# Performance work log

Measured on AMD Instinct MI355X. Metric: run time of the kernel, lower is better.

The kernel has to match this reference:

```python
import jax, jax.numpy as jnp
import numpy as np

L = 768          # temporal feature length
C_IN = 2048      # feature channels
NA = 10          # anchor scales per position
NC = 21          # num classes (20 + bg)
PRE_NMS = 1024   # pre-NMS top-k
POST_NMS = 128   # fixed proposal count after NMS
NMS_THR = 0.7
SCALE = 1.0      # cfg.Process.new_dilation*new_cluster/Frame
ANCHOR_SIZES = np.array([2., 4., 5., 6., 8., 9., 10., 12., 14., 16.], np.float32)


def _conv(x, w, b, pad=0):
    # x: [N,C,T], w: [O,I,K]
    y = jax.lax.conv_general_dilated(x, w, (1,), [(pad, pad)],
                                     dimension_numbers=('NCH', 'OIH', 'NCH'))
    return y + b[None, :, None]


def _lin(x, w, b):
    return x @ w.T + b


def _forward(feature, p):
    f = _conv(feature, p['w1f'], p['b1f'], 1)
    f = _conv(f, p['w2f'], p['b2f'], 1)
    x = _conv(f, p['wc1'], p['bc1'], 0)                      # [1,512,L]
    # SegmentProposal tower (relu only after conv4, as in source)
    h = _conv(x, p['sp1w'], p['sp1b'], 1)
    h = _conv(h, p['sp2w'], p['sp2b'], 1)
    h = _conv(h, p['sp3w'], p['sp3b'], 1)
    h = jax.nn.relu(_conv(h, p['sp4w'], p['sp4b'], 1))
    cls_score = _conv(h, p['spcw'], p['spcb'], 0)            # [1,2*NA,L]
    seg_pred = _conv(h, p['spsw'], p['spsb'], 0)             # [1,2*NA,L]

    def _resh(t):  # [1,2NA,L] -> [L*NA,2]  (transpose(2,1).view(B,L,C/2,2))
        return jnp.transpose(t, (0, 2, 1)).reshape(-1, 2)

    cls2 = _resh(cls_score)
    cls_prob = jax.nn.softmax(cls2, -1)
    off2 = _resh(seg_pred)

    # anchors: (center, half_len) per position per scale, position-major
    centers = (jnp.arange(L, dtype=jnp.float32) + 0.5) * SCALE
    halves = jnp.asarray(ANCHOR_SIZES) * 0.5
    a_c = jnp.repeat(centers, NA)
    a_h = jnp.tile(halves, L)
    im_info = L * SCALE

    # apply offsets: center shift + log-length scale, clip to video extent
    c = a_c + off2[:, 0] * (2.0 * a_h)
    hl = a_h * jnp.exp(off2[:, 1])
    s = jnp.clip(c - hl, 0.0, im_info)
    e = jnp.clip(c + hl, 0.0, im_info)
    scores = cls_prob[:, 1]

    top_sc, top_i = jax.lax.top_k(scores, PRE_NMS)
    ss, ee = s[top_i], e[top_i]

    def body(i, keep):
        inter = jnp.maximum(0., jnp.minimum(ee, ee[i]) - jnp.maximum(ss, ss[i]))
        union = (ee - ss) + (ee[i] - ss[i]) - inter
        iou = inter / jnp.maximum(union, 1e-8)
        sup = (iou > NMS_THR) & (jnp.arange(PRE_NMS) > i) & keep[i]
        return keep & ~sup

    keep = jax.lax.fori_loop(0, PRE_NMS, body, jnp.ones(PRE_NMS, bool))
    order = jnp.argsort((~keep).astype(jnp.int32), stable=True)  # kept first, score order
    sel = order[:POST_NMS]
    pidx = top_i[sel]
    ps, pe = s[pidx], e[pidx]
    pbbox = jnp.stack([(ps + pe) * 0.5, (pe - ps) * 0.5], -1)    # (center, half)

    # map proposals to feature index range (floor/ceil + clamp, as in source)
    st = jnp.clip(jnp.floor((pbbox[:, 0] - pbbox[:, 1]) / SCALE), 0, L - 1).astype(jnp.int32)
    en = jnp.clip(jnp.ceil((pbbox[:, 0] + pbbox[:, 1]) / SCALE), 0, L - 1).astype(jnp.int32)
    en = jnp.maximum(en, st)

    feat = f[0]                                              # [C_IN, L]
    tpos = jnp.arange(L)
    bins = jnp.arange(7)

    def roi_pool(se):  # AdaptiveMaxPool1d(7) over feat[:, s0:e0+1]
        s0, e0 = se
        ln = e0 - s0 + 1
        bs = s0 + (bins * ln) // 7
        be = s0 + ((bins + 1) * ln + 6) // 7 - 1
        m = (tpos[None, :] >= bs[:, None]) & (tpos[None, :] <= be[:, None])  # [7,L]
        v = jnp.where(m[None], feat[:, None, :], -jnp.inf)   # [C_IN,7,L]
        return v.max(-1)                                     # [C_IN,7]

    spp = jax.lax.map(roi_pool, (st, en))                    # [K,C_IN,7]

    y = _conv(spp, p['wc2'], p['bc2'], 0)
    y = _conv(y, p['w3'], p['b3'], 1)
    y = jax.nn.relu(_conv(y, p['w4'], p['b4'], 1))
    y = _conv(y, p['w5'], p['b5'], 1)
    y = jax.nn.relu(_conv(y, p['w6'], p['b6'], 1))
    y = y.reshape(y.shape[0], -1)                            # [K, 512*7]
    y = _lin(y, p['fc1w'], p['fc1b'])
    # Relation attention is computed but unused in the source forward -> omitted
    y = jax.nn.relu(y)
    y = _lin(y, p['fc2w'], p['fc2b'])
    y = _lin(y, p['fc3w'], p['fc3b'])
    obj_cls = _lin(y, p['clsw'], p['clsb'])                  # [K,NC]
    obj_off = _lin(y, p['boxw'], p['boxb']).reshape(-1, NC - 1, 2)
    cls_sel = cls2[pidx]                                     # [K,2]
    off_sel = off2[pidx]                                     # [K,2]
    return cls_sel, off_sel, obj_cls, obj_off


_PARAM_SHAPES = {
    'w1f': (2048, 2048, 3), 'b1f': (2048,),
    'w2f': (2048, 2048, 3), 'b2f': (2048,),
    'wc1': (512, 2048, 1), 'bc1': (512,),
    'sp1w': (512, 512, 3), 'sp1b': (512,),
    'sp2w': (512, 512, 3), 'sp2b': (512,),
    'sp3w': (512, 512, 3), 'sp3b': (512,),
    'sp4w': (512, 512, 3), 'sp4b': (512,),
    'spcw': (2 * NA, 512, 1), 'spcb': (2 * NA,),
    'spsw': (2 * NA, 512, 1), 'spsb': (2 * NA,),
    'wc2': (512, 2048, 1), 'bc2': (512,),
    'w3': (512, 512, 3), 'b3': (512,),
    'w4': (512, 512, 3), 'b4': (512,),
    'w5': (512, 512, 3), 'b5': (512,),
    'w6': (512, 512, 3), 'b6': (512,),
    'fc1w': (512, 512 * 7), 'fc1b': (512,),
    'fc2w': (256, 512), 'fc2b': (256,),
    'fc3w': (128, 256), 'fc3b': (128,),
    'clsw': (NC, 128), 'clsb': (NC,),
    'boxw': (2 * (NC - 1), 128), 'boxb': (2 * (NC - 1),),
}


def setup_inputs() -> dict:
    key = jax.random.key(0)
    inp = {'feature': jax.random.normal(jax.random.fold_in(key, 0), (1, C_IN, L), jnp.float32)}
    for i, (name, shp) in enumerate(sorted(_PARAM_SHAPES.items())):
        k = jax.random.fold_in(key, i + 1)
        inp[name] = jax.random.normal(k, shp, jnp.float32) * 0.02
    return inp


def reference(feature, b1f, b2f, b3, b4, b5, b6, bc1, bc2, boxb, boxw, clsb, clsw,
              fc1b, fc1w, fc2b, fc2w, fc3b, fc3w, sp1b, sp1w, sp2b, sp2w, sp3b, sp3w,
              sp4b, sp4w, spcb, spcw, spsb, spsw, w1f, w2f, w3, w4, w5, w6,
              wc1, wc2):
    p = dict(w1f=w1f, b1f=b1f, w2f=w2f, b2f=b2f, wc1=wc1, bc1=bc1,
             sp1w=sp1w, sp1b=sp1b, sp2w=sp2w, sp2b=sp2b, sp3w=sp3w, sp3b=sp3b,
             sp4w=sp4w, sp4b=sp4b, spcw=spcw, spcb=spcb, spsw=spsw, spsb=spsb,
             wc2=wc2, bc2=bc2, w3=w3, b3=b3, w4=w4, b4=b4, w5=w5, b5=b5,
             w6=w6, b6=b6, fc1w=fc1w, fc1b=fc1b, fc2w=fc2w, fc2b=fc2b,
             fc3w=fc3w, fc3b=fc3b, clsw=clsw, clsb=clsb, boxw=boxw, boxb=boxb)
    return _forward(feature, p)
```

## Files before the change

### kernel.cpp

```cpp
#include <hip/hip_runtime.h>

typedef __attribute__((ext_vector_type(8))) short short8;
typedef __attribute__((ext_vector_type(4))) float float4v;

__device__ __forceinline__ float bf(unsigned short u) {
    return __uint_as_float(((unsigned int)u) << 16);
}
__device__ __forceinline__ unsigned short f2b(float f) {
    unsigned int u = __float_as_uint(f);
    unsigned int r = (u + 0x7FFFu + ((u >> 16) & 1u)) >> 16;
    return (unsigned short)r;
}

__constant__ float c_anchors[10] = {2.f,4.f,5.f,6.f,8.f,9.f,10.f,12.f,14.f,16.f};

__global__ __launch_bounds__(256) void zeroXt_kernel(unsigned short* __restrict__ Xt, int CI) {
    int i = blockIdx.x * 256 + threadIdx.x;
    if (i < 2 * CI) {
        int row = (i >= CI) ? 769 : 0;
        int co = (i >= CI) ? (i - CI) : i;
        Xt[(size_t)row * CI + co] = 0;
        Xt[(size_t)770 * CI + (size_t)row * CI + co] = 0;
    }
}

__global__ __launch_bounds__(256) void decomp_kernel(const float* __restrict__ src,
                                                     unsigned short* __restrict__ Xt, int CI) {
    __shared__ float T[32][33];
    int l0 = blockIdx.x * 32, ci0 = blockIdx.y * 32;
    int tid = threadIdx.x;
#pragma unroll
    for (int i = 0; i < 4; i++) {
        int slot = tid + 256 * i;
        int r = slot >> 5, c = slot & 31;
        T[r][c] = src[(size_t)(ci0 + r) * 768 + l0 + c];
    }
    __syncthreads();
    unsigned short* Xh = Xt;
    unsigned short* Xl = Xt + (size_t)770 * CI;
#pragma unroll
    for (int i = 0; i < 4; i++) {
        int slot = tid + 256 * i;
        int li = slot >> 5, cc = slot & 31;
        float v = T[cc][li];
        unsigned short h = f2b(v);
        float lo = v - bf(h);
        size_t o = (size_t)(l0 + li + 1) * CI + ci0 + cc;
        Xh[o] = h;
        Xl[o] = f2b(lo);
    }
}

template <int TAPS>
__global__ __launch_bounds__(512, 6) void convmm_kernel(const float* __restrict__ W,
                                                        const unsigned short* __restrict__ Xt,
                                                        float* __restrict__ G,
                                                        int CO, int CI, int S) {
    constexpr int RS = TAPS * 32 + 8;
    __shared__ unsigned short At[2][64 * RS];
    __shared__ unsigned short Bt[2][130 * 40];
    int tid = threadIdx.x;
    int lane = tid & 63, wid = tid >> 6;
    int q = lane >> 4, ln = lane & 15;
    int co0 = blockIdx.x * 64;
    int l0 = blockIdx.y * 128;
    int s = blockIdx.z;
    int kPer = CI / S, cis = s * kPer;
    const unsigned short* Xh = Xt;
    const unsigned short* Xl = Xt + (size_t)770 * CI;

    float4v zero4 = {0.f, 0.f, 0.f, 0.f};
    float4v acc[2][2];
    acc[0][0] = zero4; acc[0][1] = zero4; acc[1][0] = zero4; acc[1][1] = zero4;

    int wave_m = (wid >> 2) * 32;
    int wave_n = (wid & 3) * 32;

    for (int kb = 0; kb < kPer; kb += 32) {
        int cib = cis + kb;
        if (TAPS == 3) {
#pragma unroll
            for (int i = 0; i < 2; i++) {
                int slot = tid + 512 * i;
                int row = slot >> 4, ci0 = (slot & 15) * 2;
                const float* wp = W + ((size_t)(co0 + row) * CI + cib + ci0) * 3;
                float fa[6];
#pragma unroll
                for (int j = 0; j < 6; j++) fa[j] = wp[j];
#pragma unroll
                for (int t = 0; t < 3; t++) {
                    unsigned short h0 = f2b(fa[t]);
                    unsigned short h1 = f2b(fa[t + 3]);
                    unsigned short e0 = f2b(fa[t] - bf(h0));
                    unsigned short e1 = f2b(fa[t + 3] - bf(h1));
                    *(unsigned int*)&At[0][row * RS + t * 32 + ci0] =
                        (unsigned int)h0 | ((unsigned int)h1 << 16);
                    *(unsigned int*)&At[1][row * RS + t * 32 + ci0] =
                        (unsigned int)e0 | ((unsigned int)e1 << 16);
                }
            }
        } else {
            int row = tid >> 3, ci0 = (tid & 7) * 4;
            float4 wv = *(const float4*)(W + (size_t)(co0 + row) * CI + cib + ci0);
            float fa[4] = {wv.x, wv.y, wv.z, wv.w};
            unsigned short h[4], e[4];
#pragma unroll
            for (int j = 0; j < 4; j++) {
                h[j] = f2b(fa[j]);
                e[j] = f2b(fa[j] - bf(h[j]));
            }
            unsigned long long hp = (unsigned long long)h[0] | ((unsigned long long)h[1] << 16) |
                                    ((unsigned long long)h[2] << 32) | ((unsigned long long)h[3] << 48);
            unsigned long long ep = (unsigned long long)e[0] | ((unsigned long long)e[1] << 16) |
                                    ((unsigned long long)e[2] << 32) | ((unsigned long long)e[3] << 48);
            *(unsigned long long*)&At[0][row * RS + ci0] = hp;
            *(unsigned long long*)&At[1][row * RS + ci0] = ep;
        }
#pragma unroll
        for (int i = 0; i < 3; i++) {
            int slot = tid + 512 * i;
            if (slot < 1040) {
                int p = slot >= 520 ? 1 : 0;
                int rem = slot - p * 520;
                int r = rem >> 2, qq = rem & 3;
                const unsigned short* src = (p ? Xl : Xh) + (size_t)(l0 + r) * CI + cib + qq * 8;
                short8 v = *(const short8*)src;
                *(short8*)&Bt[p][r * 40 + qq * 8] = v;
            }
        }
        __syncthreads();
#pragma unroll
        for (int t = 0; t < TAPS; t++) {
            int shift = (TAPS == 1) ? 1 : t;
            short8 bh[2], bl[2];
#pragma unroll
            for (int nf = 0; nf < 2; nf++) {
                int rrow = wave_n + nf * 16 + ln + shift;
                bh[nf] = *(const short8*)&Bt[0][rrow * 40 + q * 8];
                bl[nf] = *(const short8*)&Bt[1][rrow * 40 + q * 8];
            }
#pragma unroll
            for (int mf = 0; mf < 2; mf++) {
                int mrow = wave_m + mf * 16 + ln;
                short8 ah = *(const short8*)&At[0][mrow * RS + t * 32 + q * 8];
                short8 al = *(const short8*)&At[1][mrow * RS + t * 32 + q * 8];
#pragma unroll
                for (int nf = 0; nf < 2; nf++) {
                    acc[mf][nf] = __builtin_amdgcn_mfma_f32_16x16x32_bf16(ah, bh[nf], acc[mf][nf], 0, 0, 0);
                    acc[mf][nf] = __builtin_amdgcn_mfma_f32_16x16x32_bf16(ah, bl[nf], acc[mf][nf], 0, 0, 0);
                    acc[mf][nf] = __builtin_amdgcn_mfma_f32_16x16x32_bf16(al, bh[nf], acc[mf][nf], 0, 0, 0);
                }
            }
        }
        __syncthreads();
    }
    float* Gz = G + (size_t)s * CO * 768;
#pragma unroll
    for (int mf = 0; mf < 2; mf++)
#pragma unroll
        for (int nf = 0; nf < 2; nf++) {
            int col = l0 + wave_n + nf * 16 + ln;
            int rowb = co0 + wave_m + mf * 16 + q * 4;
#pragma unroll
            for (int r = 0; r < 4; r++)
                Gz[(size_t)(rowb + r) * 768 + col] = acc[mf][nf][r];
        }
}

__global__ __launch_bounds__(256) void finsum_x_kernel(const float* __restrict__ G,
                                                       const float* __restrict__ bias,
                                                       unsigned short* __restrict__ Xt,
                                                       int CO, int P) {
    __shared__ float T[64][65];
    int co0 = blockIdx.x * 64, l0 = blockIdx.y * 64;
    int tid = threadIdx.x;
#pragma unroll 1
    for (int i = 0; i < 16; i++) {
        int slot = tid + 256 * i;
        int r = slot >> 6, c = slot & 63;
        float v = bias[co0 + r];
        for (int p = 0; p < P; p++) v += G[((size_t)p * CO + co0 + r) * 768 + l0 + c];
        T[r][c] = v;
    }
    __syncthreads();
    unsigned short* Xh = Xt;
    unsigned short* Xl = Xt + (size_t)770 * CO;
#pragma unroll 1
    for (int i = 0; i < 16; i++) {
        int slot = tid + 256 * i;
        int li = slot >> 6, ci = slot & 63;
        float v = T[ci][li];
        unsigned short h = f2b(v);
        float lo = v - bf(h);
        size_t o = (size_t)(l0 + li + 1) * CO + co0 + ci;
        Xh[o] = h;
        Xl[o] = f2b(lo);
    }
}

__global__ __launch_bounds__(256) void finsum_xf_kernel(const float* __restrict__ G,
                                                        const float* __restrict__ bias,
                                                        unsigned short* __restrict__ Xt,
                                                        float* __restrict__ outF,
                                                        int CO, int P) {
    __shared__ float T[64][65];
    int co0 = blockIdx.x * 64, l0 = blockIdx.y * 64;
    int tid = threadIdx.x;
#pragma unroll 1
    for (int i = 0; i < 16; i++) {
        int slot = tid + 256 * i;
        int r = slot >> 6, c = slot & 63;
        float v = bias[co0 + r];
        for (int p = 0; p < P; p++) v += G[((size_t)p * CO + co0 + r) * 768 + l0 + c];
        T[r][c] = v;
        outF[(size_t)(co0 + r) * 768 + l0 + c] = v;
    }
    __syncthreads();
    unsigned short* Xh = Xt;
    unsigned short* Xl = Xt + (size_t)770 * CO;
#pragma unroll 1
    for (int i = 0; i < 16; i++) {
        int slot = tid + 256 * i;
        int li = slot >> 6, ci = slot & 63;
        float v = T[ci][li];
        unsigned short h = f2b(v);
        float lo = v - bf(h);
        size_t o = (size_t)(l0 + li + 1) * CO + co0 + ci;
        Xh[o] = h;
        Xl[o] = f2b(lo);
    }
}

__global__ __launch_bounds__(256) void finsum_f_kernel(const float* __restrict__ G,
                                                       const float* __restrict__ bias,
                                                       float* __restrict__ out,
                                                       int CO, int P, int relu) {
    int i = blockIdx.x * 256 + threadIdx.x;
    if (i >= CO * 768) return;
    int r = i / 768, c = i - r * 768;
    float v = bias[r];
    for (int p = 0; p < P; p++) v += G[((size_t)p * CO + r) * 768 + c];
    if (relu) v = fmaxf(v, 0.f);
    out[i] = v;
}

__global__ __launch_bounds__(256) void finalize_kernel(const float* __restrict__ part,
                                                       float* __restrict__ out,
                                                       const float* __restrict__ bias,
                                                       int RPAD, int R, int NCOLS, int S, int relu) {
    int i = blockIdx.x * 256 + threadIdx.x;
    int total = R * NCOLS;
    if (i >= total) return;
    int r = i / NCOLS;
    int c = i - r * NCOLS;
    float v = 0.f;
    for (int s = 0; s < S; s++) v += part[((size_t)s * RPAD + r) * NCOLS + c];
    v += bias[r];
    if (relu) v = fmaxf(v, 0.f);
    out[i] = v;
}

template <int MODE, int EPI>
__global__ __launch_bounds__(256) void gemm_kernel(const float* __restrict__ W,
                                                   const float* __restrict__ B,
                                                   const float* __restrict__ bias,
                                                   float* __restrict__ outF,
                                                   int R, int K, int NCOLS, int LDB, int S, int relu) {
    __shared__ __align__(16) float Bt[16][68];
    __shared__ __align__(16) float Wt[16][68];
    int tid = threadIdx.x;
    int tx = tid & 15, ty = tid >> 4;
    int r0 = blockIdx.x * 64, c0 = blockIdx.y * 64, s = blockIdx.z;
    int kPer = K / S;
    int k0s = s * kPer;
    float acc[4][4] = {};
    for (int kb = 0; kb < kPer; kb += 16) {
        int k0 = k0s + kb;
        {
            int rr = r0 + (tid >> 2);
            int q = tid & 3;
            float4 wv4 = {0.f, 0.f, 0.f, 0.f};
            if (rr < R) wv4 = *(const float4*)(W + (size_t)rr * K + k0 + q * 4);
            Wt[q * 4 + 0][tid >> 2] = wv4.x;
            Wt[q * 4 + 1][tid >> 2] = wv4.y;
            Wt[q * 4 + 2][tid >> 2] = wv4.z;
            Wt[q * 4 + 3][tid >> 2] = wv4.w;
        }
#pragma unroll
        for (int p = 0; p < 4; p++) {
            int kk = p * 4 + (tid >> 6);
            int c = tid & 63;
            int k = k0 + kk;
            int col = c0 + c;
            float v;
            if (MODE == 0) {
                v = B[(size_t)k * LDB + col];
            } else if (MODE == 1) {
                int ci = k / 3;
                int t = k - ci * 3;
                int lc = (col % 7) + t - 1;
                v = ((unsigned)lc < 7u) ? B[(size_t)ci * 896 + col + t - 1] : 0.f;
            } else {
                int co = k / 7;
                int b7 = k - co * 7;
                v = B[(size_t)co * 896 + col * 7 + b7];
            }
            Bt[kk][c] = v;
        }
        __syncthreads();
#pragma unroll
        for (int kk = 0; kk < 16; kk++) {
            float4 bv = *(const float4*)&Bt[kk][tx * 4];
            float4 wv = *(const float4*)&Wt[kk][ty * 4];
            float bb[4] = {bv.x, bv.y, bv.z, bv.w};
            float ww[4] = {wv.x, wv.y, wv.z, wv.w};
#pragma unroll
            for (int i = 0; i < 4; i++)
#pragma unroll
                for (int j = 0; j < 4; j++)
                    acc[i][j] = fmaf(ww[i], bb[j], acc[i][j]);
        }
        __syncthreads();
    }
    if (EPI == 0) {
        if (S > 1) {
#pragma unroll
            for (int i = 0; i < 4; i++) {
                int r = r0 + ty * 4 + i;
                float4 o = {acc[i][0], acc[i][1], acc[i][2], acc[i][3]};
                *(float4*)&outF[((size_t)s * R + r) * NCOLS + c0 + tx * 4] = o;
            }
        } else {
#pragma unroll
            for (int i = 0; i < 4; i++) {
                int r = r0 + ty * 4 + i;
                if (r < R) {
                    float bv = bias[r];
#pragma unroll
                    for (int j = 0; j < 4; j++) {
                        float v = acc[i][j] + bv;
                        if (relu) v = fmaxf(v, 0.f);
                        outF[(size_t)r * NCOLS + c0 + tx * 4 + j] = v;
                    }
                }
            }
        }
    } else {
#pragma unroll
        for (int i = 0; i < 4; i++) {
            int r = r0 + ty * 4 + i;
            if (r < R) {
                float bv = bias[r];
#pragma unroll
                for (int j = 0; j < 4; j++) {
                    int col = c0 + tx * 4 + j;
                    float v = acc[i][j] + bv;
                    if (EPI == 1) outF[512 + col * 21 + r] = v;
                    else outF[3200 + col * 40 + r] = v;
                }
            }
        }
    }
}

__global__ __launch_bounds__(256) void proposal_kernel(const float* __restrict__ clsS,
                                                       const float* __restrict__ segS,
                                                       float* __restrict__ cls2, float* __restrict__ off2,
                                                       float* __restrict__ scores,
                                                       float* __restrict__ sArr, float* __restrict__ eArr) {
    int i = blockIdx.x * 256 + threadIdx.x;
    if (i >= 7680) return;
    int l = i / 10;
    int a = i - l * 10;
    float c0 = clsS[(a * 2 + 0) * 768 + l];
    float c1 = clsS[(a * 2 + 1) * 768 + l];
    cls2[i * 2] = c0;
    cls2[i * 2 + 1] = c1;
    float m = fmaxf(c0, c1);
    float e0 = expf(c0 - m), e1 = expf(c1 - m);
    scores[i] = e1 / (e0 + e1);
    float o0 = segS[(a * 2 + 0) * 768 + l];
    float o1 = segS[(a * 2 + 1) * 768 + l];
    off2[i * 2] = o0;
    off2[i * 2 + 1] = o1;
    float ah = c_anchors[a] * 0.5f;
    float ac = (float)l + 0.5f;
    float c = ac + o0 * (2.f * ah);
    float hl = ah * expf(o1);
    sArr[i] = fminf(fmaxf(c - hl, 0.f), 768.f);
    eArr[i] = fminf(fmaxf(c + hl, 0.f), 768.f);
}

__global__ __launch_bounds__(1024) void sortA_kernel(const float* __restrict__ scores,
                                                     unsigned long long* __restrict__ runs) {
    __shared__ unsigned long long kk[1024];
    int tid = threadIdx.x;
    int gbase = blockIdx.x * 1024;
    int gi = gbase + tid;
    unsigned long long key = 0ull;
    if (gi < 7680) {
        unsigned int sb = __float_as_uint(scores[gi]);
        key = ((unsigned long long)sb << 32) | (unsigned long long)(0xFFFFFFFFu - (unsigned)gi);
    }
    kk[tid] = key;
    __syncthreads();
    for (int k = 2; k <= 1024; k <<= 1) {
        for (int j = k >> 1; j > 0; j >>= 1) {
            int ixj = tid ^ j;
            if (ixj > tid) {
                unsigned long long a = kk[tid], b = kk[ixj];
                bool descend = ((tid & k) == 0);
                if (descend ? (a < b) : (a > b)) { kk[tid] = b; kk[ixj] = a; }
            }
            __syncthreads();
        }
    }
    runs[gbase + tid] = kk[tid];
}

__global__ __launch_bounds__(1024) void sortB_kernel(const unsigned long long* __restrict__ runs,
                                                     const float* __restrict__ sArr, const float* __restrict__ eArr,
                                                     int* __restrict__ topI,
                                                     float* __restrict__ ss, float* __restrict__ ee) {
    __shared__ unsigned long long S[8192];
    int tid = threadIdx.x;
#pragma unroll
    for (int m = 0; m < 8; m++) S[m * 1024 + tid] = runs[m * 1024 + tid];
    __syncthreads();
#pragma unroll 1
    for (int level = 0; level < 3; level++) {
        int span = 1024 << level;
        int nm = 4 >> level;
        for (int m = 0; m < nm; m++) {
            int baseA = m * (span * 2);
            int baseB = baseA + span;
            unsigned long long a = S[baseA + tid], b = S[baseB + 1023 - tid];
            S[baseA + tid] = (a > b) ? a : b;
        }
        __syncthreads();
        for (int j = 512; j > 0; j >>= 1) {
            for (int m = 0; m < nm; m++) {
                int baseA = m * (span * 2);
                int ixj = tid ^ j;
                if (ixj > tid) {
                    unsigned long long a = S[baseA + tid], b = S[baseA + ixj];
                    if (a < b) { S[baseA + tid] = b; S[baseA + ixj] = a; }
                }
            }
            __syncthreads();
        }
    }
    int idx = (int)(0xFFFFFFFFu - (unsigned int)(S[tid] & 0xFFFFFFFFull));
    topI[tid] = idx;
    ss[tid] = sArr[idx];
    ee[tid] = eArr[idx];
}

__global__ __launch_bounds__(256) void nms_mask_kernel(const float* __restrict__ ss, const float* __restrict__ ee,
                                                       unsigned long long* __restrict__ mask) {
    int g = blockIdx.x * 256 + threadIdx.x;
    int i = g >> 4, w = g & 15;
    float si = ss[i], ei = ee[i];
    unsigned long long bits = 0ull;
#pragma unroll 1
    for (int jj = 0; jj < 64; jj++) {
        int j = w * 64 + jj;
        if (j > i) {
            float sj = ss[j], ej = ee[j];
            float inter = fmaxf(0.f, fminf(ei, ej) - fmaxf(si, sj));
            float uni = (ej - sj) + (ei - si) - inter;
            float iou = inter / fmaxf(uni, 1e-8f);
            if (iou > 0.7f) bits |= (1ull << jj);
        }
    }
    mask[(size_t)i * 16 + w] = bits;
}

__device__ __forceinline__ unsigned long long readlane64(unsigned long long v, int i) {
    unsigned int lo = (unsigned int)__builtin_amdgcn_readlane((int)(unsigned int)(v & 0xFFFFFFFFull), i);
    unsigned int hi = (unsigned int)__builtin_amdgcn_readlane((int)(unsigned int)(v >> 32), i);
    return ((unsigned long long)hi << 32) | (unsigned long long)lo;
}

__global__ __launch_bounds__(64) void nms_select_kernel(const unsigned long long* __restrict__ mask,
                                                        const int* __restrict__ topI,
                                                        const float* __restrict__ ss, const float* __restrict__ ee,
                                                        const float* __restrict__ cls2, const float* __restrict__ off2,
                                                        int* __restrict__ stA, int* __restrict__ enA,
                                                        float* __restrict__ out) {
    int lane = threadIdx.x;
    unsigned long long keepW[16];
#pragma unroll 1
    for (int b = 0; b < 16; b++) {
        unsigned long long accv = 0ull;
#pragma unroll 1
        for (int a = 0; a < b; a++) {
            unsigned long long m = mask[(size_t)(a * 64 + lane) * 16 + b];
            unsigned long long kb = (keepW[a] >> lane) & 1ull;
            accv |= m & (0ull - kb);
        }
#pragma unroll
        for (int sft = 1; sft < 64; sft <<= 1) accv |= __shfl_xor(accv, sft);
        unsigned long long diag = mask[(size_t)(b * 64 + lane) * 16 + b];
        unsigned long long rem = accv;
#pragma unroll
        for (int i = 0; i < 64; i++) {
            unsigned long long di = readlane64(diag, i);
            if (!((rem >> i) & 1ull)) rem |= di;
        }
        keepW[b] = ~rem;
    }
    int total = 0;
    int prefix[16];
#pragma unroll
    for (int b = 0; b < 16; b++) { prefix[b] = total; total += __popcll(keepW[b]); }
#pragma unroll 1
    for (int b = 0; b < 16; b++) {
        int tid = b * 64 + lane;
        unsigned long long keep64 = keepW[b];
        unsigned long long below = (lane == 0) ? 0ull : (keep64 << (64 - lane));
        int keptBefore = prefix[b] + __popcll(below);
        int kp = (int)((keep64 >> lane) & 1ull);
        int pos = kp ? keptBefore : (total + tid - keptBefore);
        if (pos < 128) {
            int orig = topI[tid];
            float ps = ss[tid], pe = ee[tid];
            out[pos * 2 + 0] = cls2[orig * 2 + 0];
            out[pos * 2 + 1] = cls2[orig * 2 + 1];
            out[256 + pos * 2 + 0] = off2[orig * 2 + 0];
            out[256 + pos * 2 + 1] = off2[orig * 2 + 1];
            float bc = (ps + pe) * 0.5f, bh = (pe - ps) * 0.5f;
            int st = (int)fminf(fmaxf(floorf(bc - bh), 0.f), 767.f);
            int en = (int)fminf(fmaxf(ceilf(bc + bh), 0.f), 767.f);
            if (en < st) en = st;
            stA[pos] = st;
            enA[pos] = en;
        }
    }
}

__global__ __launch_bounds__(256) void roi_kernel(const float* __restrict__ f,
                                                  const int* __restrict__ stA, const int* __restrict__ enA,
                                                  float* __restrict__ spp) {
    int n = blockIdx.x;
    int c = blockIdx.y * 256 + threadIdx.x;
    int st = stA[n], en = enA[n];
    int ln = en - st + 1;
    const float* row = f + (size_t)c * 768;
#pragma unroll 1
    for (int b = 0; b < 7; b++) {
        int bs = st + (b * ln) / 7;
        int be = st + ((b + 1) * ln + 6) / 7 - 1;
        float m = row[bs];
        for (int t = bs + 1; t <= be; t++) m = fmaxf(m, row[t]);
        spp[(size_t)c * 896 + n * 7 + b] = m;
    }
}

extern "C" void kernel_launch(void* const* d_in, const int* in_sizes, int n_in,
                              void* d_out, int out_size, void* d_ws, size_t ws_size,
                              hipStream_t stream) {
    const float* IN[39];
    for (int i = 0; i < 39; i++) IN[i] = (const float*)d_in[i];
    const float* feature = IN[0];
    const float *b1f = IN[1], *b2f = IN[2], *b3 = IN[3], *b4 = IN[4], *b5 = IN[5], *b6 = IN[6];
    const float *bc1 = IN[7], *bc2 = IN[8], *boxb = IN[9], *boxw = IN[10];
    const float *clsb = IN[11], *clsw = IN[12];
    const float *fc1b = IN[13], *fc1w = IN[14], *fc2b = IN[15], *fc2w = IN[16];
    const float *fc3b = IN[17], *fc3w = IN[18];
    const float *sp1b = IN[19], *sp1w = IN[20], *sp2b = IN[21], *sp2w = IN[22];
    const float *sp3b = IN[23], *sp3w = IN[24], *sp4b = IN[25], *sp4w = IN[26];
    const float *spcb = IN[27], *spcw = IN[28], *spsb = IN[29], *spsw = IN[30];
    const float *w1f = IN[31], *w2f = IN[32], *w3w = IN[33], *w4w = IN[34];
    const float *w5w = IN[35], *w6w = IN[36], *wc1 = IN[37], *wc2 = IN[38];
    float* out = (float*)d_out;

    char* base = (char*)d_ws;
    float* G    = (float*)base;
    float* part = (float*)base;
    float* spp  = (float*)(base + 14680064);
    float* yA   = (float*)(base + 22020096);
    float* yB   = (float*)(base + 23855104);
    float* g1   = (float*)(base + 25690112);
    float* g2   = (float*)(base + 25952256);
    float* g3   = (float*)(base + 26083328);
    size_t off = 26148864;
    auto alloc = [&](size_t bytes) { void* p = base + off; off += (bytes + 15) & ~((size_t)15); return p; };
    unsigned short* Xt = (unsigned short*)alloc((size_t)770 * 2048 * 2 * 2);
    float* fbuf = (float*)alloc((size_t)2048 * 768 * 4);
    float* hB   = (float*)alloc((size_t)512 * 768 * 4);
    float* clsS = (float*)alloc((size_t)20 * 768 * 4);
    float* segS = (float*)alloc((size_t)20 * 768 * 4);
    float* cls2 = (float*)alloc(7680 * 2 * 4);
    float* off2 = (float*)alloc(7680 * 2 * 4);
    float* scores = (float*)alloc(7680 * 4);
    float* sArr = (float*)alloc(7680 * 4);
    float* eArr = (float*)alloc(7680 * 4);
    float* ssS  = (float*)alloc(1024 * 4);
    float* eeS  = (float*)alloc(1024 * 4);
    unsigned long long* runs = (unsigned long long*)alloc((size_t)8192 * 8);
    unsigned long long* mask = (unsigned long long*)alloc((size_t)16384 * 8);
    int* topI = (int*)alloc(1024 * 4);
    int* stA = (int*)alloc(128 * 4);
    int* enA = (int*)alloc(128 * 4);

    dim3 blk(256);
    dim3 blk512(512);

    zeroXt_kernel<<<16, blk, 0, stream>>>(Xt, 2048);
    decomp_kernel<<<dim3(24, 64), blk, 0, stream>>>(feature, Xt, 2048);
    convmm_kernel<3><<<dim3(32, 6, 4), blk512, 0, stream>>>(w1f, Xt, G, 2048, 2048, 4);
    finsum_x_kernel<<<dim3(32, 12), blk, 0, stream>>>(G, b1f, Xt, 2048, 4);
    convmm_kernel<3><<<dim3(32, 6, 4), blk512, 0, stream>>>(w2f, Xt, G, 2048, 2048, 4);
    finsum_xf_kernel<<<dim3(32, 12), blk, 0, stream>>>(G, b2f, Xt, fbuf, 2048, 4);

    convmm_kernel<1><<<dim3(8, 6, 8), blk512, 0, stream>>>(wc1, Xt, G, 512, 2048, 8);
    zeroXt_kernel<<<4, blk, 0, stream>>>(Xt, 512);
    finsum_x_kernel<<<dim3(8, 12), blk, 0, stream>>>(G, bc1, Xt, 512, 8);

    convmm_kernel<3><<<dim3(8, 6, 8), blk512, 0, stream>>>(sp1w, Xt, G, 512, 512, 8);
    finsum_x_kernel<<<dim3(8, 12), blk, 0, stream>>>(G, sp1b, Xt, 512, 8);
    convmm_kernel<3><<<dim3(8, 6, 8), blk512, 0, stream>>>(sp2w, Xt, G, 512, 512, 8);
    finsum_x_kernel<<<dim3(8, 12), blk, 0, stream>>>(G, sp2b, Xt, 512, 8);
    convmm_kernel<3><<<dim3(8, 6, 8), blk512, 0, stream>>>(sp3w, Xt, G, 512, 512, 8);
    finsum_x_kernel<<<dim3(8, 12), blk, 0, stream>>>(G, sp3b, Xt, 512, 8);
    convmm_kernel<3><<<dim3(8, 6, 8), blk512, 0, stream>>>(sp4w, Xt, G, 512, 512, 8);
    finsum_f_kernel<<<1536, blk, 0, stream>>>(G, sp4b, hB, 512, 8, 1);

    gemm_kernel<0, 0><<<dim3(1, 12, 1), blk, 0, stream>>>(spcw, hB, spcb, clsS, 20, 512, 768, 768, 1, 0);
    gemm_kernel<0, 0><<<dim3(1, 12, 1), blk, 0, stream>>>(spsw, hB, spsb, segS, 20, 512, 768, 768, 1, 0);

    proposal_kernel<<<30, blk, 0, stream>>>(clsS, segS, cls2, off2, scores, sArr, eArr);
    sortA_kernel<<<8, 1024, 0, stream>>>(scores, runs);
    sortB_kernel<<<1, 1024, 0, stream>>>(runs, sArr, eArr, topI, ssS, eeS);
    nms_mask_kernel<<<64, blk, 0, stream>>>(ssS, eeS, mask);
    nms_select_kernel<<<1, 64, 0, stream>>>(mask, topI, ssS, eeS, cls2, off2, stA, enA, out);

    roi_kernel<<<dim3(128, 8), blk, 0, stream>>>(fbuf, stA, enA, spp);

    gemm_kernel<0, 0><<<dim3(8, 14, 8), blk, 0, stream>>>(wc2, spp, bc2, part, 512, 2048, 896, 896, 8, 0);
    finalize_kernel<<<1792, blk, 0, stream>>>(part, yA, bc2, 512, 512, 896, 8, 0);

    gemm_kernel<1, 0><<<dim3(8, 14, 8), blk, 0, stream>>>(w3w, yA, b3, part, 512, 1536, 896, 896, 8, 0);
    finalize_kernel<<<1792, blk, 0, stream>>>(part, yB, b3, 512, 512, 896, 8, 0);
    gemm_kernel<1, 0><<<dim3(8, 14, 8), blk, 0, stream>>>(w4w, yB, b4, part, 512, 1536, 896, 896, 8, 0);
    finalize_kernel<<<1792, blk, 0, stream>>>(part, yA, b4, 512, 512, 896, 8, 1);
    gemm_kernel<1, 0><<<dim3(8, 14, 8), blk, 0, stream>>>(w5w, yA, b5, part, 512, 1536, 896, 896, 8, 0);
    finalize_kernel<<<1792, blk, 0, stream>>>(part, yB, b5, 512, 512, 896, 8, 0);
    gemm_kernel<1, 0><<<dim3(8, 14, 8), blk, 0, stream>>>(w6w, yB, b6, part, 512, 1536, 896, 896, 8, 0);
    finalize_kernel<<<1792, blk, 0, stream>>>(part, yA, b6, 512, 512, 896, 8, 1);

    gemm_kernel<2, 0><<<dim3(8, 2, 28), blk, 0, stream>>>(fc1w, yA, fc1b, part, 512, 3584, 128, 128, 28, 0);
    finalize_kernel<<<256, blk, 0, stream>>>(part, g1, fc1b, 512, 512, 128, 28, 1);

    gemm_kernel<0, 0><<<dim3(4, 2, 4), blk, 0, stream>>>(fc2w, g1, fc2b, part, 256, 512, 128, 128, 4, 0);
    finalize_kernel<<<128, blk, 0, stream>>>(part, g2, fc2b, 256, 256, 128, 4, 0);
    gemm_kernel<0, 0><<<dim3(2, 2, 2), blk, 0, stream>>>(fc3w, g2, fc3b, part, 128, 256, 128, 128, 2, 0);
    finalize_kernel<<<64, blk, 0, stream>>>(part, g3, fc3b, 128, 128, 128, 2, 0);

    gemm_kernel<0, 1><<<dim3(1, 2, 1), blk, 0, stream>>>(clsw, g3, clsb, out, 21, 128, 128, 128, 1, 0);
    gemm_kernel<0, 2><<<dim3(1, 2, 1), blk, 0, stream>>>(boxw, g3, boxb, out, 40, 128, 128, 128, 1, 0);
}
```

Before: 1.065 ms.

## Run RoI head convs through split-bf16 MFMA conv kernel with padded segment layout

Moves the post-RoI 1x1 and 3-tap convolution stack (wc2, w3..w6) off the generic scalar gemm_kernel and onto the MFMA-based convmm_kernel. A SEGM template mode maps each 7-bin proposal segment to a 9-row padded slab, so the 3-tap conv reads zero halos without boundary checks. The RoI pooling now writes bf16 hi/lo pairs directly into the transposed slab, and new finsum kernels write the next layer in the same padded format. This adds zeroing kernels and more index arithmetic, and relies on split-bf16 (hi/lo, three products) accuracy matching the fp32 path.

New measurement: 1.029 ms. 3.3% less time.

```diff
diff --git a/kernel.cpp b/kernel.cpp
--- a/kernel.cpp
+++ b/kernel.cpp
@@ -51,23 +51,25 @@
     }
 }
 
-template <int TAPS>
+template <int TAPS, int SEGM>
 __global__ __launch_bounds__(512, 6) void convmm_kernel(const float* __restrict__ W,
                                                         const unsigned short* __restrict__ Xt,
                                                         float* __restrict__ G,
-                                                        int CO, int CI, int S) {
+                                                        int CO, int CI, int S, int NCOL, int planeElems) {
     constexpr int RS = TAPS * 32 + 8;
+    constexpr int BROWS = SEGM ? 168 : 130;
     __shared__ unsigned short At[2][64 * RS];
-    __shared__ unsigned short Bt[2][130 * 40];
+    __shared__ unsigned short Bt[2][BROWS * 40];
     int tid = threadIdx.x;
     int lane = tid & 63, wid = tid >> 6;
     int q = lane >> 4, ln = lane & 15;
     int co0 = blockIdx.x * 64;
-    int l0 = blockIdx.y * 128;
+    int c0 = blockIdx.y * 128;
     int s = blockIdx.z;
     int kPer = CI / S, cis = s * kPer;
     const unsigned short* Xh = Xt;
-    const unsigned short* Xl = Xt + (size_t)770 * CI;
+    const unsigned short* Xl = Xt + planeElems;
+    int row0 = SEGM ? ((c0 / 7) * 9 + c0 % 7) : c0;
 
     float4v zero4 = {0.f, 0.f, 0.f, 0.f};
     float4v acc[2][2];
@@ -76,14 +78,21 @@
     int wave_m = (wid >> 2) * 32;
     int wave_n = (wid & 3) * 32;
 
+    int rowb[2];
+#pragma unroll
+    for (int nf = 0; nf < 2; nf++) {
+        int col = c0 + wave_n + nf * 16 + ln;
+        rowb[nf] = SEGM ? ((col / 7) * 9 + col % 7 - row0) : (wave_n + nf * 16 + ln);
+    }
+
     for (int kb = 0; kb < kPer; kb += 32) {
         int cib = cis + kb;
         if (TAPS == 3) {
 #pragma unroll
             for (int i = 0; i < 2; i++) {
                 int slot = tid + 512 * i;
-                int row = slot >> 4, ci0 = (slot & 15) * 2;
-                const float* wp = W + ((size_t)(co0 + row) * CI + cib + ci0) * 3;
+                int row = slot >> 4, cc0 = (slot & 15) * 2;
+                const float* wp = W + ((size_t)(co0 + row) * CI + cib + cc0) * 3;
                 float fa[6];
 #pragma unroll
                 for (int j = 0; j < 6; j++) fa[j] = wp[j];
@@ -93,15 +102,15 @@
                     unsigned short h1 = f2b(fa[t + 3]);
                     unsigned short e0 = f2b(fa[t] - bf(h0));
                     unsigned short e1 = f2b(fa[t + 3] - bf(h1));
-                    *(unsigned int*)&At[0][row * RS + t * 32 + ci0] =
+                    *(unsigned int*)&At[0][row * RS + t * 32 + cc0] =
                         (unsigned int)h0 | ((unsigned int)h1 << 16);
-                    *(unsigned int*)&At[1][row * RS + t * 32 + ci0] =
+                    *(unsigned int*)&At[1][row * RS + t * 32 + cc0] =
                         (unsigned int)e0 | ((unsigned int)e1 << 16);
                 }
             }
         } else {
-            int row = tid >> 3, ci0 = (tid & 7) * 4;
-            float4 wv = *(const float4*)(W + (size_t)(co0 + row) * CI + cib + ci0);
+            int row = tid >> 3, cc0 = (tid & 7) * 4;
+            float4 wv = *(const float4*)(W + (size_t)(co0 + row) * CI + cib + cc0);
             float fa[4] = {wv.x, wv.y, wv.z, wv.w};
             unsigned short h[4], e[4];
 #pragma unroll
@@ -113,17 +122,17 @@
                                     ((unsigned long long)h[2] << 32) | ((unsigned long long)h[3] << 48);
             unsigned long long ep = (unsigned long long)e[0] | ((unsigned long long)e[1] << 16) |
                                     ((unsigned long long)e[2] << 32) | ((unsigned long long)e[3] << 48);
-            *(unsigned long long*)&At[0][row * RS + ci0] = hp;
-            *(unsigned long long*)&At[1][row * RS + ci0] = ep;
+            *(unsigned long long*)&At[0][row * RS + cc0] = hp;
+            *(unsigned long long*)&At[1][row * RS + cc0] = ep;
         }
 #pragma unroll
         for (int i = 0; i < 3; i++) {
             int slot = tid + 512 * i;
-            if (slot < 1040) {
-                int p = slot >= 520 ? 1 : 0;
-                int rem = slot - p * 520;
+            if (slot < BROWS * 8) {
+                int p = slot >= BROWS * 4 ? 1 : 0;
+                int rem = slot - p * BROWS * 4;
                 int r = rem >> 2, qq = rem & 3;
-                const unsigned short* src = (p ? Xl : Xh) + (size_t)(l0 + r) * CI + cib + qq * 8;
+                const unsigned short* src = (p ? Xl : Xh) + (size_t)(row0 + r) * CI + cib + qq * 8;
                 short8 v = *(const short8*)src;
                 *(short8*)&Bt[p][r * 40 + qq * 8] = v;
             }
@@ -135,7 +144,7 @@
             short8 bh[2], bl[2];
 #pragma unroll
             for (int nf = 0; nf < 2; nf++) {
-                int rrow = wave_n + nf * 16 + ln + shift;
+                int rrow = rowb[nf] + shift;
                 bh[nf] = *(const short8*)&Bt[0][rrow * 40 + q * 8];
                 bl[nf] = *(const short8*)&Bt[1][rrow * 40 + q * 8];
             }
@@ -154,16 +163,16 @@
         }
         __syncthreads();
     }
-    float* Gz = G + (size_t)s * CO * 768;
+    float* Gz = G + (size_t)s * CO * NCOL;
 #pragma unroll
     for (int mf = 0; mf < 2; mf++)
 #pragma unroll
         for (int nf = 0; nf < 2; nf++) {
-            int col = l0 + wave_n + nf * 16 + ln;
-            int rowb = co0 + wave_m + mf * 16 + q * 4;
+            int col = c0 + wave_n + nf * 16 + ln;
+            int rowb2 = co0 + wave_m + mf * 16 + q * 4;
 #pragma unroll
             for (int r = 0; r < 4; r++)
-                Gz[(size_t)(rowb + r) * 768 + col] = acc[mf][nf][r];
+                Gz[(size_t)(rowb2 + r) * NCOL + col] = acc[mf][nf][r];
         }
 }
 
@@ -231,15 +240,49 @@
     }
 }
 
+__global__ __launch_bounds__(256) void finsum_seg_kernel(const float* __restrict__ G,
+                                                         const float* __restrict__ bias,
+                                                         unsigned short* __restrict__ Xs,
+                                                         int P, int relu) {
+    __shared__ float T[64][65];
+    int co0 = blockIdx.x * 64, c0 = blockIdx.y * 64;
+    int tid = threadIdx.x;
+#pragma unroll 1
+    for (int i = 0; i < 16; i++) {
+        int slot = tid + 256 * i;
+        int r = slot >> 6, c = slot & 63;
+        float v = bias[co0 + r];
+        for (int p = 0; p < P; p++) v += G[((size_t)p * 512 + co0 + r) * 896 + c0 + c];
+        if (relu) v = fmaxf(v, 0.f);
+        T[r][c] = v;
+    }
+    __syncthreads();
+    unsigned short* Xh = Xs;
+    unsigned short* Xl = Xs + (size_t)1160 * 512;
+#pragma unroll 1
+    for (int i = 0; i < 16; i++) {
+        int slot = tid + 256 * i;
+        int li = slot >> 6, ci = slot & 63;
+        float v = T[ci][li];
+        int c = c0 + li;
+        int row = (c / 7) * 9 + c % 7 + 1;
+        unsigned short h = f2b(v);
+        float lo = v - bf(h);
+        size_t o = (size_t)row * 512 + co0 + ci;
+        Xh[o] = h;
+        Xl[o] = f2b(lo);
+    }
+}
+
 __global__ __launch_bounds__(256) void finsum_f_kernel(const float* __restrict__ G,
                                                        const float* __restrict__ bias,
                                                        float* __restrict__ out,
-                                                       int CO, int P, int relu) {
+                                                       int CO, int P, int ncol, int relu) {
     int i = blockIdx.x * 256 + threadIdx.x;
-    if (i >= CO * 768) return;
-    int r = i / 768, c = i - r * 768;
+    if (i >= CO * ncol) return;
+    int r = i / ncol, c = i - r * ncol;
     float v = bias[r];
-    for (int p = 0; p < P; p++) v += G[((size_t)p * CO + r) * 768 + c];
+    for (int p = 0; p < P; p++) v += G[((size_t)p * CO + r) * ncol + c];
     if (relu) v = fmaxf(v, 0.f);
     out[i] = v;
 }
@@ -295,11 +338,6 @@
             float v;
             if (MODE == 0) {
                 v = B[(size_t)k * LDB + col];
-            } else if (MODE == 1) {
-                int ci = k / 3;
-                int t = k - ci * 3;
-                int lc = (col % 7) + t - 1;
-                v = ((unsigned)lc < 7u) ? B[(size_t)ci * 896 + col + t - 1] : 0.f;
             } else {
                 int co = k / 7;
                 int b7 = k - co * 7;
@@ -539,22 +577,46 @@
     }
 }
 
-__global__ __launch_bounds__(256) void roi_kernel(const float* __restrict__ f,
-                                                  const int* __restrict__ stA, const int* __restrict__ enA,
-                                                  float* __restrict__ spp) {
-    int n = blockIdx.x;
-    int c = blockIdx.y * 256 + threadIdx.x;
+__global__ __launch_bounds__(256) void roi_slab_kernel(const float* __restrict__ f,
+                                                       const int* __restrict__ stA, const int* __restrict__ enA,
+                                                       unsigned short* __restrict__ Xs) {
+    int col = blockIdx.x;
+    int n = col / 7, b = col - n * 7;
     int st = stA[n], en = enA[n];
     int ln = en - st + 1;
-    const float* row = f + (size_t)c * 768;
-#pragma unroll 1
-    for (int b = 0; b < 7; b++) {
-        int bs = st + (b * ln) / 7;
-        int be = st + ((b + 1) * ln + 6) / 7 - 1;
+    int bs = st + (b * ln) / 7;
+    int be = st + ((b + 1) * ln + 6) / 7 - 1;
+    unsigned short* Xh = Xs;
+    unsigned short* Xl = Xs + (size_t)898 * 2048;
+    int tid = threadIdx.x;
+#pragma unroll 1
+    for (int j = 0; j < 8; j++) {
+        int ci = tid + 256 * j;
+        const float* row = f + (size_t)ci * 768;
         float m = row[bs];
         for (int t = bs + 1; t <= be; t++) m = fmaxf(m, row[t]);
-        spp[(size_t)c * 896 + n * 7 + b] = m;
-    }
+        unsigned short h = f2b(m);
+        float lo = m - bf(h);
+        size_t o = (size_t)(col + 1) * 2048 + ci;
+        Xh[o] = h;
+        Xl[o] = f2b(lo);
+    }
+}
+
+__global__ __launch_bounds__(256) void zrow_wc2_kernel(unsigned short* __restrict__ Xs) {
+    int i = blockIdx.x * 256 + threadIdx.x;
+    if (i < 2048) {
+        Xs[i] = 0;
+        Xs[(size_t)897 * 2048 + i] = 0;
+        Xs[(size_t)898 * 2048 + i] = 0;
+        Xs[(size_t)898 * 2048 + (size_t)897 * 2048 + i] = 0;
+    }
+}
+
+__global__ __launch_bounds__(256) void zseg_kernel(uint4* __restrict__ p, int n16) {
+    int i = blockIdx.x * 256 + threadIdx.x;
+    uint4 z = {0, 0, 0, 0};
+    if (i < n16) p[i] = z;
 }
 
 extern "C" void kernel_launch(void* const* d_in, const int* in_sizes, int n_in,
@@ -578,9 +640,9 @@
     char* base = (char*)d_ws;
     float* G    = (float*)base;
     float* part = (float*)base;
-    float* spp  = (float*)(base + 14680064);
+    unsigned short* segSA = (unsigned short*)(base + 14680064);
+    unsigned short* segSB = (unsigned short*)(base + 17055744);
     float* yA   = (float*)(base + 22020096);
-    float* yB   = (float*)(base + 23855104);
     float* g1   = (float*)(base + 25690112);
     float* g2   = (float*)(base + 25952256);
     float* g3   = (float*)(base + 26083328);
@@ -609,23 +671,23 @@
 
     zeroXt_kernel<<<16, blk, 0, stream>>>(Xt, 2048);
     decomp_kernel<<<dim3(24, 64), blk, 0, stream>>>(feature, Xt, 2048);
-    convmm_kernel<3><<<dim3(32, 6, 4), blk512, 0, stream>>>(w1f, Xt, G, 2048, 2048, 4);
+    convmm_kernel<3, 0><<<dim3(32, 6, 4), blk512, 0, stream>>>(w1f, Xt, G, 2048, 2048, 4, 768, 770 * 2048);
     finsum_x_kernel<<<dim3(32, 12), blk, 0, stream>>>(G, b1f, Xt, 2048, 4);
-    convmm_kernel<3><<<dim3(32, 6, 4), blk512, 0, stream>>>(w2f, Xt, G, 2048, 2048, 4);
+    convmm_kernel<3, 0><<<dim3(32, 6, 4), blk512, 0, stream>>>(w2f, Xt, G, 2048, 2048, 4, 768, 770 * 2048);
     finsum_xf_kernel<<<dim3(32, 12), blk, 0, stream>>>(G, b2f, Xt, fbuf, 2048, 4);
 
-    convmm_kernel<1><<<dim3(8, 6, 8), blk512, 0, stream>>>(wc1, Xt, G, 512, 2048, 8);
+    convmm_kernel<1, 0><<<dim3(8, 6, 8), blk512, 0, stream>>>(wc1, Xt, G, 512, 2048, 8, 768, 770 * 2048);
     zeroXt_kernel<<<4, blk, 0, stream>>>(Xt, 512);
     finsum_x_kernel<<<dim3(8, 12), blk, 0, stream>>>(G, bc1, Xt, 512, 8);
 
-    convmm_kernel<3><<<dim3(8, 6, 8), blk512, 0, stream>>>(sp1w, Xt, G, 512, 512, 8);
+    convmm_kernel<3, 0><<<dim3(8, 6, 8), blk512, 0, stream>>>(sp1w, Xt, G, 512, 512, 8, 768, 770 * 512);
     finsum_x_kernel<<<dim3(8, 12), blk, 0, stream>>>(G, sp1b, Xt, 512, 8);
-    convmm_kernel<3><<<dim3(8, 6, 8), blk512, 0, stream>>>(sp2w, Xt, G, 512, 512, 8);
+    convmm_kernel<3, 0><<<dim3(8, 6, 8), blk512, 0, stream>>>(sp2w, Xt, G, 512, 512, 8, 768, 770 * 512);
     finsum_x_kernel<<<dim3(8, 12), blk, 0, stream>>>(G, sp2b, Xt, 512, 8);
-    convmm_kernel<3><<<dim3(8, 6, 8), blk512, 0, stream>>>(sp3w, Xt, G, 512, 512, 8);
+    convmm_kernel<3, 0><<<dim3(8, 6, 8), blk512, 0, stream>>>(sp3w, Xt, G, 512, 512, 8, 768, 770 * 512);
     finsum_x_kernel<<<dim3(8, 12), blk, 0, stream>>>(G, sp3b, Xt, 512, 8);
-    convmm_kernel<3><<<dim3(8, 6, 8), blk512, 0, stream>>>(sp4w, Xt, G, 512, 512, 8);
-    finsum_f_kernel<<<1536, blk, 0, stream>>>(G, sp4b, hB, 512, 8, 1);
+    convmm_kernel<3, 0><<<dim3(8, 6, 8), blk512, 0, stream>>>(sp4w, Xt, G, 512, 512, 8, 768, 770 * 512);
+    finsum_f_kernel<<<1536, blk, 0, stream>>>(G, sp4b, hB, 512, 8, 768, 1);
 
     gemm_kernel<0, 0><<<dim3(1, 12, 1), blk, 0, stream>>>(spcw, hB, spcb, clsS, 20, 512, 768, 768, 1, 0);
     gemm_kernel<0, 0><<<dim3(1, 12, 1), blk, 0, stream>>>(spsw, hB, spsb, segS, 20, 512, 768, 768, 1, 0);
@@ -636,21 +698,22 @@
     nms_mask_kernel<<<64, blk, 0, stream>>>(ssS, eeS, mask);
     nms_select_kernel<<<1, 64, 0, stream>>>(mask, topI, ssS, eeS, cls2, off2, stA, enA, out);
 
-    roi_kernel<<<dim3(128, 8), blk, 0, stream>>>(fbuf, stA, enA, spp);
-
-    gemm_kernel<0, 0><<<dim3(8, 14, 8), blk, 0, stream>>>(wc2, spp, bc2, part, 512, 2048, 896, 896, 8, 0);
-    finalize_kernel<<<1792, blk, 0, stream>>>(part, yA, bc2, 512, 512, 896, 8, 0);
-
-    gemm_kernel<1, 0><<<dim3(8, 14, 8), blk, 0, stream>>>(w3w, yA, b3, part, 512, 1536, 896, 896, 8, 0);
-    finalize_kernel<<<1792, blk, 0, stream>>>(part, yB, b3, 512, 512, 896, 8, 0);
-    gemm_kernel<1, 0><<<dim3(8, 14, 8), blk, 0, stream>>>(w4w, yB, b4, part, 512, 1536, 896, 896, 8, 0);
-    finalize_kernel<<<1792, blk, 0, stream>>>(part, yA, b4, 512, 512, 896, 8, 1);
-    gemm_kernel<1, 0><<<dim3(8, 14, 8), blk, 0, stream>>>(w5w, yA, b5, part, 512, 1536, 896, 896, 8, 0);
-    finalize_kernel<<<1792, blk, 0, stream>>>(part, yB, b5, 512, 512, 896, 8, 0);
-    gemm_kernel<1, 0><<<dim3(8, 14, 8), blk, 0, stream>>>(w6w, yB, b6, part, 512, 1536, 896, 896, 8, 0);
-    finalize_kernel<<<1792, blk, 0, stream>>>(part, yA, b6, 512, 512, 896, 8, 1);
-
-    gemm_kernel<2, 0><<<dim3(8, 2, 28), blk, 0, stream>>>(fc1w, yA, fc1b, part, 512, 3584, 128, 128, 28, 0);
+    zrow_wc2_kernel<<<8, blk, 0, stream>>>(Xt);
+    roi_slab_kernel<<<896, blk, 0, stream>>>(fbuf, stA, enA, Xt);
+    zseg_kernel<<<1160, blk, 0, stream>>>((uint4*)segSA, 296960);
+
+    convmm_kernel<1, 0><<<dim3(8, 7, 8), blk512, 0, stream>>>(wc2, Xt, G, 512, 2048, 8, 896, 898 * 2048);
+    finsum_seg_kernel<<<dim3(8, 14), blk, 0, stream>>>(G, bc2, segSA, 8, 0);
+    convmm_kernel<3, 1><<<dim3(8, 7, 8), blk512, 0, stream>>>(w3w, segSA, G, 512, 512, 8, 896, 1160 * 512);
+    finsum_seg_kernel<<<dim3(8, 14), blk, 0, stream>>>(G, b3, segSB, 8, 0);
+    convmm_kernel<3, 1><<<dim3(8, 7, 8), blk512, 0, stream>>>(w4w, segSB, G, 512, 512, 8, 896, 1160 * 512);
+    finsum_seg_kernel<<<dim3(8, 14), blk, 0, stream>>>(G, b4, segSA, 8, 1);
+    convmm_kernel<3, 1><<<dim3(8, 7, 8), blk512, 0, stream>>>(w5w, segSA, G, 512, 512, 8, 896, 1160 * 512);
+    finsum_seg_kernel<<<dim3(8, 14), blk, 0, stream>>>(G, b5, segSB, 8, 0);
+    convmm_kernel<3, 1><<<dim3(8, 7, 8), blk512, 0, stream>>>(w6w, segSB, G, 512, 512, 8, 896, 1160 * 512);
+    finsum_f_kernel<<<1792, blk, 0, stream>>>(G, b6, yA, 512, 8, 896, 1);
+
+    gemm_kernel<1, 0><<<dim3(8, 2, 28), blk, 0, stream>>>(fc1w, yA, fc1b, part, 512, 3584, 128, 128, 28, 0);
     finalize_kernel<<<256, blk, 0, stream>>>(part, g1, fc1b, 512, 512, 128, 28, 1);
 
     gemm_kernel<0, 0><<<dim3(4, 2, 4), blk, 0, stream>>>(fc2w, g1, fc2b, part, 256, 512, 128, 128, 4, 0);
```
